# Performance work log

Measured on AMD Instinct MI355X. Metric: run time of the kernel, lower is better.

Reference implementation:

```python
import jax, jax.numpy as jnp
import numpy as np

B, S, E, H = 2, 2048, 1024, 8
DH = E // H          # v head dim = 128
F = DH // 2          # q/k sub-head dim = 64


def setup_inputs() -> dict:
    key = jax.random.key(0)
    ks = jax.random.split(key, 7)
    sc = E ** -0.5
    return {
        "x": jax.random.normal(ks[0], (B, S, E), dtype=jnp.float32),
        "Wq": jax.random.normal(ks[1], (E, E), dtype=jnp.float32) * sc,
        "Wk": jax.random.normal(ks[2], (E, E), dtype=jnp.float32) * sc,
        "Wv": jax.random.normal(ks[3], (E, E), dtype=jnp.float32) * sc,
        "norm_w": jnp.ones((H, DH), dtype=jnp.float32),
        "Wo": jax.random.normal(ks[4], (E, E), dtype=jnp.float32) * sc,
        "bo": jnp.zeros((E,), dtype=jnp.float32),
        "diff_weight": jnp.float32(0.2),
    }


def reference(x, Wq, Wk, Wv, norm_w, Wo, bo, diff_weight):
    b, s, e = x.shape
    # projections (Linear with weight [out,in] -> x @ W.T)
    qs = (x @ Wq.T).reshape(b, s, H, 2, F)
    ks_ = (x @ Wk.T).reshape(b, s, H, 2, F)
    vs = (x @ Wv.T).reshape(b, s, H, DH)
    scale = F ** -0.5
    # two attention branches: [2, b, h, q, k]
    scores = jnp.einsum('bqhif,bkhif->ibhqk', qs, ks_) * scale
    atts = jax.nn.softmax(scores, axis=-1)
    att = atts[0] - diff_weight * atts[1]          # [b,h,q,k]
    o = jnp.einsum('bhqk,bkhe->bqhe', att, vs)     # [b,q,h,dh]
    # RMSNorm over the joint (heads, head_dim) dims, as in nn.RMSNorm([H, DH])
    eps = jnp.finfo(o.dtype).eps
    rms = jax.lax.rsqrt(jnp.mean(o * o, axis=(-2, -1), keepdims=True) + eps)
    normed = (o * rms * norm_w).reshape(b, s, e)
    return (normed @ Wo.T + bo) * (1.0 - diff_weight)
```

## Files before the change

### kernel.cpp

```cpp
#include <hip/hip_runtime.h>
#include <hip/hip_bf16.h>
#include <math.h>


#define SDIM 2048
#define EDIM 1024
#define HDIM 8
#define DHDIM 128

typedef unsigned short u16;
typedef __attribute__((ext_vector_type(8))) short bf16x8;
typedef __attribute__((ext_vector_type(4))) short bf16x4;
typedef __attribute__((ext_vector_type(4))) u16 u16x4;
typedef __attribute__((ext_vector_type(8))) u16 u16x8;
typedef __attribute__((ext_vector_type(4))) float f32x4;

__device__ __forceinline__ u16 bf16rne(float f) {
    unsigned int u = __float_as_uint(f);
    u += 0x7fff + ((u >> 16) & 1);
    return (u16)(u >> 16);
}

__device__ __forceinline__ void gload16(void* lds, const void* g) {
    __builtin_amdgcn_global_load_lds(
        (const __attribute__((address_space(1))) unsigned int*)g,
        (__attribute__((address_space(3))) unsigned int*)lds, 16, 0, 0);
}

constexpr int GM = 4096, GN = 1024, GK = 1024;

__global__ __launch_bounds__(256) void cast_bf16(
    const float* __restrict__ x,  const float* __restrict__ wq,
    const float* __restrict__ wk, const float* __restrict__ wv,
    const float* __restrict__ wo,
    u16* __restrict__ xb,  u16* __restrict__ wqb, u16* __restrict__ wkb,
    u16* __restrict__ wvb, u16* __restrict__ wob)
{
    int bid = blockIdx.x;
    const float* src; u16* dst; int lb;
    if (bid < 2048)      { src = x;  dst = xb;  lb = bid; }
    else if (bid < 2560) { src = wq; dst = wqb; lb = bid - 2048; }
    else if (bid < 3072) { src = wk; dst = wkb; lb = bid - 2560; }
    else if (bid < 3584) { src = wv; dst = wvb; lb = bid - 3072; }
    else                 { src = wo; dst = wob; lb = bid - 3584; }
    size_t i = ((size_t)lb * 256 + threadIdx.x) * 8;
    float4 a = *(const float4*)&src[i];
    float4 b = *(const float4*)&src[i + 4];
    u16x8 o;
    o[0] = bf16rne(a.x); o[1] = bf16rne(a.y); o[2] = bf16rne(a.z); o[3] = bf16rne(a.w);
    o[4] = bf16rne(b.x); o[5] = bf16rne(b.y); o[6] = bf16rne(b.z); o[7] = bf16rne(b.w);
    *(u16x8*)&dst[i] = o;
}

struct GemmCore {
    f32x4 acc[4][4];
    int m0, n0, wm, wn, ln, quad;
};

__device__ __forceinline__ void gemm_swz(GemmCore& g) {
    const int bid = blockIdx.y * gridDim.x + blockIdx.x;
    const int cpx = (gridDim.x * gridDim.y) >> 3;
    const int swz = (bid & 7) * cpx + (bid >> 3);
    g.m0 = (swz / gridDim.x) * 128;
    g.n0 = (swz % gridDim.x) * 128;
}

#define QBUF 4096

__device__ __forceinline__ void gemm_core32(
    GemmCore& g, const u16* __restrict__ A, const u16* __restrict__ W,
    u16* AsBase, u16* BsBase)
{
    const int tid = threadIdx.x;
    const int lane = tid & 63;
    const int wv = tid >> 6;
    g.ln = lane & 15; g.quad = lane >> 4;
    g.wm = (wv >> 1) * 64; g.wn = (wv & 1) * 64;
    gemm_swz(g);

#pragma unroll
    for (int i = 0; i < 4; ++i)
#pragma unroll
        for (int j = 0; j < 4; ++j)
            g.acc[i][j] = (f32x4){0.f, 0.f, 0.f, 0.f};

    const int s0 = tid, s1 = tid + 256;
    const int ar0 = s0 >> 2, ac0 = (((s0 & 3) ^ ((ar0 >> 1) & 3)) * 8);
    const int ar1 = s1 >> 2, ac1 = (((s1 & 3) ^ ((ar1 >> 1) & 3)) * 8);
    const u16* pa0 = A + (size_t)(g.m0 + ar0) * GK + ac0;
    const u16* pa1 = A + (size_t)(g.m0 + ar1) * GK + ac1;
    const u16* pb0 = W + (size_t)(g.n0 + ar0) * GK + ac0;
    const u16* pb1 = W + (size_t)(g.n0 + ar1) * GK + ac1;
    u16* la0 = AsBase + s0 * 8; u16* la1 = AsBase + s1 * 8;
    u16* lb0 = BsBase + s0 * 8; u16* lb1 = BsBase + s1 * 8;

    const int roff = ((g.quad ^ ((g.ln >> 1) & 3)) * 8);

    gload16(la0, pa0); gload16(la1, pa1);
    gload16(lb0, pb0); gload16(lb1, pb1);

    for (int k0 = 0; k0 < GK; k0 += 32) {
        const int cur = (k0 >> 5) & 1;
        __syncthreads();

        if (k0 + 32 < GK) {
            const int nb = (cur ^ 1) * QBUF;
            gload16(la0 + nb, pa0 + k0 + 32); gload16(la1 + nb, pa1 + k0 + 32);
            gload16(lb0 + nb, pb0 + k0 + 32); gload16(lb1 + nb, pb1 + k0 + 32);
        }

        const u16* Ac = AsBase + cur * QBUF;
        const u16* Bc = BsBase + cur * QBUF;

        bf16x8 af[4], bfr[4];
#pragma unroll
        for (int t = 0; t < 4; ++t) {
            af[t]  = *(const bf16x8*)&Ac[(g.wm + t * 16 + g.ln) * 32 + roff];
            bfr[t] = *(const bf16x8*)&Bc[(g.wn + t * 16 + g.ln) * 32 + roff];
        }
#pragma unroll
        for (int i = 0; i < 4; ++i)
#pragma unroll
            for (int j = 0; j < 4; ++j)
                g.acc[i][j] = __builtin_amdgcn_mfma_f32_16x16x32_bf16(
                    af[i], bfr[j], g.acc[i][j], 0, 0, 0);
    }
}

#define GBUF 8192

__device__ __forceinline__ void gemm_core64(
    GemmCore& g, const u16* __restrict__ A, const u16* __restrict__ W,
    u16* AsBase, u16* BsBase)
{
    const int tid = threadIdx.x;
    const int lane = tid & 63;
    const int wv = tid >> 6;
    g.ln = lane & 15; g.quad = lane >> 4;
    g.wm = (wv >> 1) * 64; g.wn = (wv & 1) * 64;
    gemm_swz(g);

#pragma unroll
    for (int i = 0; i < 4; ++i)
#pragma unroll
        for (int j = 0; j < 4; ++j)
            g.acc[i][j] = (f32x4){0.f, 0.f, 0.f, 0.f};

    const int s0 = tid, s1 = tid + 256, s2 = tid + 512, s3 = tid + 768;
    const int ar0 = s0 >> 3, ac0 = ((s0 & 7) ^ (ar0 & 7)) * 8;
    const int ar1 = s1 >> 3, ac1 = ((s1 & 7) ^ (ar1 & 7)) * 8;
    const int ar2 = s2 >> 3, ac2 = ((s2 & 7) ^ (ar2 & 7)) * 8;
    const int ar3 = s3 >> 3, ac3 = ((s3 & 7) ^ (ar3 & 7)) * 8;
    const u16* pa0 = A + (size_t)(g.m0 + ar0) * GK + ac0;
    const u16* pa1 = A + (size_t)(g.m0 + ar1) * GK + ac1;
    const u16* pa2 = A + (size_t)(g.m0 + ar2) * GK + ac2;
    const u16* pa3 = A + (size_t)(g.m0 + ar3) * GK + ac3;
    const u16* pb0 = W + (size_t)(g.n0 + ar0) * GK + ac0;
    const u16* pb1 = W + (size_t)(g.n0 + ar1) * GK + ac1;
    const u16* pb2 = W + (size_t)(g.n0 + ar2) * GK + ac2;
    const u16* pb3 = W + (size_t)(g.n0 + ar3) * GK + ac3;
    u16* la0 = AsBase + s0 * 8; u16* la1 = AsBase + s1 * 8;
    u16* la2 = AsBase + s2 * 8; u16* la3 = AsBase + s3 * 8;
    u16* lb0 = BsBase + s0 * 8; u16* lb1 = BsBase + s1 * 8;
    u16* lb2 = BsBase + s2 * 8; u16* lb3 = BsBase + s3 * 8;

    gload16(la0, pa0); gload16(la1, pa1);
    gload16(la2, pa2); gload16(la3, pa3);
    gload16(lb0, pb0); gload16(lb1, pb1);
    gload16(lb2, pb2); gload16(lb3, pb3);

    for (int k0 = 0; k0 < GK; k0 += 64) {
        const int cur = (k0 >> 6) & 1;
        __syncthreads();

        if (k0 + 64 < GK) {
            const int nb = (cur ^ 1) * GBUF;
            gload16(la0 + nb, pa0 + k0 + 64); gload16(la1 + nb, pa1 + k0 + 64);
            gload16(la2 + nb, pa2 + k0 + 64); gload16(la3 + nb, pa3 + k0 + 64);
            gload16(lb0 + nb, pb0 + k0 + 64); gload16(lb1 + nb, pb1 + k0 + 64);
            gload16(lb2 + nb, pb2 + k0 + 64); gload16(lb3 + nb, pb3 + k0 + 64);
        }

        const u16* Ac = AsBase + cur * GBUF;
        const u16* Bc = BsBase + cur * GBUF;

        bf16x8 af[4][2], bfr[4][2];
#pragma unroll
        for (int t = 0; t < 4; ++t) {
#pragma unroll
            for (int kk = 0; kk < 2; ++kk) {
                const int ra = g.wm + t * 16 + g.ln;
                const int rb = g.wn + t * 16 + g.ln;
                af[t][kk]  = *(const bf16x8*)&Ac[ra * 64 + (((kk * 4 + g.quad) ^ (ra & 7)) * 8)];
                bfr[t][kk] = *(const bf16x8*)&Bc[rb * 64 + (((kk * 4 + g.quad) ^ (rb & 7)) * 8)];
            }
        }
#pragma unroll
        for (int i = 0; i < 4; ++i)
#pragma unroll
            for (int j = 0; j < 4; ++j)
#pragma unroll
                for (int kk = 0; kk < 2; ++kk)
                    g.acc[i][j] = __builtin_amdgcn_mfma_f32_16x16x32_bf16(
                        af[i][kk], bfr[j][kk], g.acc[i][j], 0, 0, 0);
    }
}

#define TSTR 136

__global__ __launch_bounds__(256) void gemm_qkv(
    const u16* __restrict__ A,
    const u16* __restrict__ W0, const u16* __restrict__ W1, const u16* __restrict__ W2,
    u16* __restrict__ Qb, u16* __restrict__ Kb, u16* __restrict__ Vtb)
{
    __shared__ u16 Sh[17408];
    const int z = blockIdx.z;
    const u16* W = (z == 0) ? W0 : ((z == 1) ? W1 : W2);
    GemmCore g;
    gemm_core32(g, A, W, Sh, Sh + 2 * QBUF);

    if (z < 2) {
        const float scl = (z == 0) ? 0.125f * 1.44269504f : 1.0f;
        u16* C = (z == 0) ? Qb : Kb;
#pragma unroll
        for (int i = 0; i < 4; ++i) {
            int rb = g.m0 + g.wm + i * 16 + g.quad * 4;
#pragma unroll
            for (int r = 0; r < 4; ++r) {
                u16* crow = C + (size_t)(rb + r) * GN + g.n0 + g.wn + g.ln;
#pragma unroll
                for (int j = 0; j < 4; ++j)
                    crow[j * 16] = bf16rne(g.acc[i][j][r] * scl);
            }
        }
    } else {
        __syncthreads();
        u16* Ts = Sh;
#pragma unroll
        for (int i = 0; i < 4; ++i)
#pragma unroll
            for (int j = 0; j < 4; ++j) {
                const int nl = g.wn + j * 16 + g.ln;
                const int ml = g.wm + i * 16 + g.quad * 4;
                u16x4 pk;
#pragma unroll
                for (int r = 0; r < 4; ++r) pk[r] = bf16rne(g.acc[i][j][r]);
                *(u16x4*)&Ts[nl * TSTR + ml] = pk;
            }
        __syncthreads();

        const int tid = threadIdx.x;
        const int c = tid & 15;
        const int bb = g.m0 >> 11;
        const int sb0 = g.m0 & 2047;
        const int hh = g.n0 >> 7;
#pragma unroll
        for (int s = 0; s < 8; ++s) {
            const int rown = (tid >> 4) + s * 16;
            u16x8 v = *(const u16x8*)&Ts[rown * TSTR + c * 8];
            u16* vrow = Vtb + (((size_t)bb * 8 + hh) * DHDIM + rown) * SDIM + sb0;
            *(u16x8*)&vrow[c * 8] = v;
        }
    }
}

__global__ __launch_bounds__(256) void gemm_out(
    const u16* __restrict__ A, const u16* __restrict__ W,
    float* __restrict__ C, const float* __restrict__ bias,
    const float* __restrict__ dwp)
{
    __shared__ u16 Sh[4 * GBUF];
    GemmCore g;
    gemm_core64(g, A, W, Sh, Sh + 2 * GBUF);

    const float scale = 1.0f - dwp[0];
    float bv[4];
#pragma unroll
    for (int j = 0; j < 4; ++j) bv[j] = bias[g.n0 + g.wn + j * 16 + g.ln];
#pragma unroll
    for (int i = 0; i < 4; ++i) {
        int rb = g.m0 + g.wm + i * 16 + g.quad * 4;
#pragma unroll
        for (int r = 0; r < 4; ++r) {
            float* crow = C + (size_t)(rb + r) * GN + g.n0 + g.wn + g.ln;
#pragma unroll
            for (int j = 0; j < 4; ++j)
                crow[j * 16] = (g.acc[i][j][r] + bv[j]) * scale;
        }
    }
}

#define KBUF 4096
#define VBUF 8192

__global__ __launch_bounds__(256, 2) void attn_mfma(
    const u16* __restrict__ Qb, const u16* __restrict__ Kb,
    const u16* __restrict__ Vtb,
    float* __restrict__ Oacc, float* __restrict__ Lacc)
{
    __shared__ u16 Ks[2 * KBUF];
    __shared__ u16 Vs[2 * VBUF];

    const int tid = threadIdx.x;
    const int wv   = tid >> 6;
    const int lane = tid & 63;
    const int ln = lane & 15, quad = lane >> 4;
    const int lx = ln & 7;
    const int vkey = (ln >> 1) & 3;
    const int bh = blockIdx.y, b = bh >> 3, h = bh & 7;
    const int q0 = blockIdx.x * 128 + wv * 32;
    const int BR = blockIdx.z;

    const size_t qoff = (size_t)b * SDIM * EDIM + h * DHDIM + BR * 64;
    bf16x8 aq[2][2];
#pragma unroll
    for (int qt = 0; qt < 2; ++qt) {
        const u16* qp = Qb + qoff + (size_t)(q0 + qt * 16 + ln) * EDIM + quad * 8;
        aq[qt][0] = *(const bf16x8*)(qp);
        aq[qt][1] = *(const bf16x8*)(qp + 32);
    }

    const int s0 = tid, s1 = tid + 256;
    const int kr0 = s0 >> 3, kc0 = ((s0 & 7) ^ (kr0 & 7)) * 8;
    const int kr1 = s1 >> 3, kc1 = ((s1 & 7) ^ (kr1 & 7)) * 8;
    const u16* kg0 = Kb + (size_t)(b * SDIM + kr0) * EDIM + h * DHDIM + BR * 64 + kc0;
    const u16* kg1 = Kb + (size_t)(b * SDIM + kr1) * EDIM + h * DHDIM + BR * 64 + kc1;
    const int vr0 = s0 >> 2, vc0 = ((s0 & 3) ^ ((vr0 >> 1) & 3)) * 8;
    const int vr1 = s1 >> 2, vc1 = ((s1 & 3) ^ ((vr1 >> 1) & 3)) * 8;
    const u16* vg0 = Vtb + ((size_t)bh * DHDIM + vr0) * SDIM + vc0;
    const u16* vg1 = Vtb + ((size_t)bh * DHDIM + vr1) * SDIM + vc1;
    u16* ksd0 = Ks + s0 * 8; u16* ksd1 = Ks + s1 * 8;
    u16* vsd0 = Vs + s0 * 8; u16* vsd1 = Vs + s1 * 8;

    gload16(ksd0, kg0); gload16(ksd1, kg1);
    gload16(vsd0, vg0); gload16(vsd1, vg1);
    gload16(vsd0 + 4096, vg0 + 32); gload16(vsd1 + 4096, vg1 + 32);
    kg0 += 64 * EDIM; kg1 += 64 * EDIM; vg0 += 64; vg1 += 64;

    f32x4 acc[2][8];
#pragma unroll
    for (int qt = 0; qt < 2; ++qt)
#pragma unroll
        for (int d = 0; d < 8; ++d)
            acc[qt][d] = (f32x4){0.f, 0.f, 0.f, 0.f};
    float lsum[2] = {0.f, 0.f};
    const f32x4 z4 = (f32x4){0.f, 0.f, 0.f, 0.f};

    for (int it = 0; it < 32; ++it) {
        const int cur = it & 1;
        __syncthreads();

        if (it < 31) {
            const int kb = (cur ^ 1) * KBUF, vb2 = (cur ^ 1) * VBUF;
            gload16(ksd0 + kb, kg0); gload16(ksd1 + kb, kg1);
            gload16(vsd0 + vb2, vg0); gload16(vsd1 + vb2, vg1);
            gload16(vsd0 + vb2 + 4096, vg0 + 32); gload16(vsd1 + vb2 + 4096, vg1 + 32);
            kg0 += 64 * EDIM; kg1 += 64 * EDIM; vg0 += 64; vg1 += 64;
        }

        const u16* Kc = Ks + cur * KBUF;
        const u16* Vc = Vs + cur * VBUF;

        bf16x8 kf[4][2];
#pragma unroll
        for (int t2 = 0; t2 < 4; ++t2) {
            const int rb = (t2 * 16 + ln) * 64;
            kf[t2][0] = *(const bf16x8*)&Kc[rb + ((quad ^ lx) * 8)];
            kf[t2][1] = *(const bf16x8*)&Kc[rb + (((4 + quad) ^ lx) * 8)];
        }

        f32x4 st[2][4];
#pragma unroll
        for (int t2 = 0; t2 < 4; ++t2)
#pragma unroll
            for (int qt = 0; qt < 2; ++qt) {
                f32x4 s = __builtin_amdgcn_mfma_f32_16x16x32_bf16(kf[t2][0], aq[qt][0], z4, 0, 0, 0);
                st[qt][t2] = __builtin_amdgcn_mfma_f32_16x16x32_bf16(kf[t2][1], aq[qt][1], s, 0, 0, 0);
            }

        bf16x8 vf[8][2];
#pragma unroll
        for (int dt = 0; dt < 8; ++dt) {
            const int vb = (dt * 16 + ln) * 32;
#pragma unroll
            for (int ks = 0; ks < 2; ++ks) {
                const u16* Vk = Vc + ks * 4096;
                bf16x4 vlo = *(const bf16x4*)&Vk[vb + ((((quad >> 1) + 0) ^ vkey) * 8 + (quad & 1) * 4)];
                bf16x4 vhi = *(const bf16x4*)&Vk[vb + ((((quad >> 1) + 2) ^ vkey) * 8 + (quad & 1) * 4)];
                vf[dt][ks] = __builtin_shufflevector(vlo, vhi, 0, 1, 2, 3, 4, 5, 6, 7);
            }
        }

        union { unsigned int u[4]; bf16x8 v; } ap[2][2];
#pragma unroll
        for (int qt = 0; qt < 2; ++qt)
#pragma unroll
            for (int ks = 0; ks < 2; ++ks) {
                float e0 = exp2f(st[qt][2 * ks][0]), e1 = exp2f(st[qt][2 * ks][1]);
                float e2 = exp2f(st[qt][2 * ks][2]), e3 = exp2f(st[qt][2 * ks][3]);
                float f0 = exp2f(st[qt][2 * ks + 1][0]), f1 = exp2f(st[qt][2 * ks + 1][1]);
                float f2 = exp2f(st[qt][2 * ks + 1][2]), f3 = exp2f(st[qt][2 * ks + 1][3]);
                lsum[qt] += (e0 + e1) + (e2 + e3) + (f0 + f1) + (f2 + f3);
                ap[qt][ks].u[0] = __builtin_amdgcn_perm(__float_as_uint(e1), __float_as_uint(e0), 0x07060302u);
                ap[qt][ks].u[1] = __builtin_amdgcn_perm(__float_as_uint(e3), __float_as_uint(e2), 0x07060302u);
                ap[qt][ks].u[2] = __builtin_amdgcn_perm(__float_as_uint(f1), __float_as_uint(f0), 0x07060302u);
                ap[qt][ks].u[3] = __builtin_amdgcn_perm(__float_as_uint(f3), __float_as_uint(f2), 0x07060302u);
            }

#pragma unroll
        for (int dt = 0; dt < 8; ++dt)
#pragma unroll
            for (int ks = 0; ks < 2; ++ks)
#pragma unroll
                for (int qt = 0; qt < 2; ++qt)
                    acc[qt][dt] = __builtin_amdgcn_mfma_f32_16x16x32_bf16(ap[qt][ks].v, vf[dt][ks], acc[qt][dt], 0, 0, 0);
    }

#pragma unroll
    for (int qt = 0; qt < 2; ++qt) {
#pragma unroll
        for (int r = 0; r < 4; ++r) {
            size_t row = (size_t)(b * SDIM + q0 + qt * 16 + quad * 4 + r);
            float* o = Oacc + ((row * 8 + h) * 2 + BR) * 128 + ln;
#pragma unroll
            for (int dt = 0; dt < 8; ++dt)
                o[dt * 16] = acc[qt][dt][r];
        }
    }
#pragma unroll
    for (int qt = 0; qt < 2; ++qt) {
        float l = lsum[qt];
        l += __shfl_xor(l, 16, 64); l += __shfl_xor(l, 32, 64);
        if (quad == 0)
            Lacc[(size_t)((b * 8 + h) * 2 + BR) * SDIM + q0 + qt * 16 + ln] = l;
    }
}

__global__ __launch_bounds__(256) void rms_combine(
    const float* __restrict__ Oacc, const float* __restrict__ Lacc,
    const float* __restrict__ nw, u16* __restrict__ Nb,
    const float* __restrict__ dwp)
{
    const int row = blockIdx.x;
    const int tid = threadIdx.x;
    const int h = tid >> 5, dh0 = (tid & 31) * 4;
    const int b = row >> 11, q = row & 2047;

    size_t ob = ((size_t)row * 8 + h) * 2 * 128;
    f32x4 a0 = *(const f32x4*)&Oacc[ob + dh0];
    f32x4 a1 = *(const f32x4*)&Oacc[ob + 128 + dh0];
    float l0 = Lacc[(size_t)((b * 8 + h) * 2 + 0) * SDIM + q];
    float l1 = Lacc[(size_t)((b * 8 + h) * 2 + 1) * SDIM + q];
    const float dw = dwp[0];
    float inv0 = 1.0f / l0;
    float inv1 = dw / l1;
    float o[4];
#pragma unroll
    for (int k = 0; k < 4; ++k) o[k] = a0[k] * inv0 - a1[k] * inv1;

    float ss = o[0] * o[0] + o[1] * o[1] + o[2] * o[2] + o[3] * o[3];
    ss += __shfl_xor(ss, 1,  64);
    ss += __shfl_xor(ss, 2,  64);
    ss += __shfl_xor(ss, 4,  64);
    ss += __shfl_xor(ss, 8,  64);
    ss += __shfl_xor(ss, 16, 64);
    ss += __shfl_xor(ss, 32, 64);
    __shared__ float red[4];
    if ((tid & 63) == 0) red[tid >> 6] = ss;
    __syncthreads();
    float tot = red[0] + red[1] + red[2] + red[3];
    float rms = rsqrtf(tot * (1.0f / 1024.0f) + 1.1920929e-07f);

    float4 w = *(const float4*)&nw[tid * 4];
    u16x4 pk;
    pk[0] = bf16rne(o[0] * rms * w.x);
    pk[1] = bf16rne(o[1] * rms * w.y);
    pk[2] = bf16rne(o[2] * rms * w.z);
    pk[3] = bf16rne(o[3] * rms * w.w);
    *(u16x4*)&Nb[(size_t)row * EDIM + tid * 4] = pk;
}

extern "C" void kernel_launch(void* const* d_in, const int* in_sizes, int n_in,
                              void* d_out, int out_size, void* d_ws, size_t ws_size,
                              hipStream_t stream)
{
    const float* x   = (const float*)d_in[0];
    const float* Wq  = (const float*)d_in[1];
    const float* Wk  = (const float*)d_in[2];
    const float* Wv  = (const float*)d_in[3];
    const float* nw  = (const float*)d_in[4];
    const float* Wo  = (const float*)d_in[5];
    const float* bo  = (const float*)d_in[6];
    const float* dwp = (const float*)d_in[7];
    float* out = (float*)d_out;

    float* Oacc = (float*)d_ws;
    u16*  xb   = (u16*)d_ws;
    u16*  wob  = (u16*)((char*)d_ws + 33554432);
    u16*  wqb  = wob + 1048576;
    u16*  wkb  = wqb + 1048576;
    u16*  wvb  = wkb + 1048576;
    float* Lacc = (float*)wqb;
    u16*  Qb   = wvb + 1048576;
    u16*  Kb   = Qb + 4194304;
    u16*  Vtb  = Kb + 4194304;
    u16*  Nb   = Qb;

    cast_bf16<<<4096, 256, 0, stream>>>(x, Wq, Wk, Wv, Wo,
                                        xb, wqb, wkb, wvb, wob);
    gemm_qkv<<<dim3(GN / 128, GM / 128, 3), 256, 0, stream>>>(
        xb, wqb, wkb, wvb, Qb, Kb, Vtb);
    attn_mfma<<<dim3(SDIM / 128, 2 * HDIM, 2), 256, 0, stream>>>(
        Qb, Kb, Vtb, Oacc, Lacc);
    rms_combine<<<4096, 256, 0, stream>>>(Oacc, Lacc, nw, Nb, dwp);
    gemm_out<<<dim3(GN / 128, GM / 128, 1), 256, 0, stream>>>(
        Nb, wob, out, bo, dwp);
}
```

Before: 212.9 us.

## Fuse fp32-to-bf16 cast of x into QKV GEMM A-tile loading

Drops the separate bf16 cast of the activation x. The QKV GEMM now reads fp32 x directly through registers, converts it, and stores bf16 into LDS with software prefetch across the MFMA loop. This removes one pass of writing and re-reading x as bf16. In exchange, each of the 3 z-slices and every N-tile re-reads fp32 x at twice the bytes, and the A loads lose the async global-to-LDS path.

```diff
diff --git a/kernel.cpp b/kernel.cpp
--- a/kernel.cpp
+++ b/kernel.cpp
@@ -27,29 +27,31 @@
         (__attribute__((address_space(3))) unsigned int*)lds, 16, 0, 0);
 }
 
+__device__ __forceinline__ u16x8 cvt8(float4 a, float4 b) {
+    u16x8 o;
+    o[0] = bf16rne(a.x); o[1] = bf16rne(a.y); o[2] = bf16rne(a.z); o[3] = bf16rne(a.w);
+    o[4] = bf16rne(b.x); o[5] = bf16rne(b.y); o[6] = bf16rne(b.z); o[7] = bf16rne(b.w);
+    return o;
+}
+
 constexpr int GM = 4096, GN = 1024, GK = 1024;
 
 __global__ __launch_bounds__(256) void cast_bf16(
-    const float* __restrict__ x,  const float* __restrict__ wq,
-    const float* __restrict__ wk, const float* __restrict__ wv,
-    const float* __restrict__ wo,
-    u16* __restrict__ xb,  u16* __restrict__ wqb, u16* __restrict__ wkb,
+    const float* __restrict__ wq, const float* __restrict__ wk,
+    const float* __restrict__ wv, const float* __restrict__ wo,
+    u16* __restrict__ wqb, u16* __restrict__ wkb,
     u16* __restrict__ wvb, u16* __restrict__ wob)
 {
     int bid = blockIdx.x;
     const float* src; u16* dst; int lb;
-    if (bid < 2048)      { src = x;  dst = xb;  lb = bid; }
-    else if (bid < 2560) { src = wq; dst = wqb; lb = bid - 2048; }
-    else if (bid < 3072) { src = wk; dst = wkb; lb = bid - 2560; }
-    else if (bid < 3584) { src = wv; dst = wvb; lb = bid - 3072; }
-    else                 { src = wo; dst = wob; lb = bid - 3584; }
+    if (bid < 512)       { src = wq; dst = wqb; lb = bid; }
+    else if (bid < 1024) { src = wk; dst = wkb; lb = bid - 512; }
+    else if (bid < 1536) { src = wv; dst = wvb; lb = bid - 1024; }
+    else                 { src = wo; dst = wob; lb = bid - 1536; }
     size_t i = ((size_t)lb * 256 + threadIdx.x) * 8;
     float4 a = *(const float4*)&src[i];
     float4 b = *(const float4*)&src[i + 4];
-    u16x8 o;
-    o[0] = bf16rne(a.x); o[1] = bf16rne(a.y); o[2] = bf16rne(a.z); o[3] = bf16rne(a.w);
-    o[4] = bf16rne(b.x); o[5] = bf16rne(b.y); o[6] = bf16rne(b.z); o[7] = bf16rne(b.w);
-    *(u16x8*)&dst[i] = o;
+    *(u16x8*)&dst[i] = cvt8(a, b);
 }
 
 struct GemmCore {
@@ -67,8 +69,8 @@
 
 #define QBUF 4096
 
-__device__ __forceinline__ void gemm_core32(
-    GemmCore& g, const u16* __restrict__ A, const u16* __restrict__ W,
+__device__ __forceinline__ void gemm_core32f(
+    GemmCore& g, const float* __restrict__ X, const u16* __restrict__ W,
     u16* AsBase, u16* BsBase)
 {
     const int tid = threadIdx.x;
@@ -87,8 +89,8 @@
     const int s0 = tid, s1 = tid + 256;
     const int ar0 = s0 >> 2, ac0 = (((s0 & 3) ^ ((ar0 >> 1) & 3)) * 8);
     const int ar1 = s1 >> 2, ac1 = (((s1 & 3) ^ ((ar1 >> 1) & 3)) * 8);
-    const u16* pa0 = A + (size_t)(g.m0 + ar0) * GK + ac0;
-    const u16* pa1 = A + (size_t)(g.m0 + ar1) * GK + ac1;
+    const float* xa0 = X + (size_t)(g.m0 + ar0) * GK + ac0;
+    const float* xa1 = X + (size_t)(g.m0 + ar1) * GK + ac1;
     const u16* pb0 = W + (size_t)(g.n0 + ar0) * GK + ac0;
     const u16* pb1 = W + (size_t)(g.n0 + ar1) * GK + ac1;
     u16* la0 = AsBase + s0 * 8; u16* la1 = AsBase + s1 * 8;
@@ -96,16 +98,28 @@
 
     const int roff = ((g.quad ^ ((g.ln >> 1) & 3)) * 8);
 
-    gload16(la0, pa0); gload16(la1, pa1);
+    {
+        float4 a0 = *(const float4*)(xa0);
+        float4 a1 = *(const float4*)(xa0 + 4);
+        float4 b0 = *(const float4*)(xa1);
+        float4 b1 = *(const float4*)(xa1 + 4);
+        *(u16x8*)la0 = cvt8(a0, a1);
+        *(u16x8*)la1 = cvt8(b0, b1);
+    }
     gload16(lb0, pb0); gload16(lb1, pb1);
 
     for (int k0 = 0; k0 < GK; k0 += 32) {
         const int cur = (k0 >> 5) & 1;
         __syncthreads();
 
-        if (k0 + 32 < GK) {
+        const bool pf = (k0 + 32 < GK);
+        float4 na0, na1, nb0l, nb1l;
+        if (pf) {
+            na0  = *(const float4*)(xa0 + k0 + 32);
+            na1  = *(const float4*)(xa0 + k0 + 36);
+            nb0l = *(const float4*)(xa1 + k0 + 32);
+            nb1l = *(const float4*)(xa1 + k0 + 36);
             const int nb = (cur ^ 1) * QBUF;
-            gload16(la0 + nb, pa0 + k0 + 32); gload16(la1 + nb, pa1 + k0 + 32);
             gload16(lb0 + nb, pb0 + k0 + 32); gload16(lb1 + nb, pb1 + k0 + 32);
         }
 
@@ -124,6 +138,12 @@
             for (int j = 0; j < 4; ++j)
                 g.acc[i][j] = __builtin_amdgcn_mfma_f32_16x16x32_bf16(
                     af[i], bfr[j], g.acc[i][j], 0, 0, 0);
+
+        if (pf) {
+            const int nb = (cur ^ 1) * QBUF;
+            *(u16x8*)(la0 + nb) = cvt8(na0, na1);
+            *(u16x8*)(la1 + nb) = cvt8(nb0l, nb1l);
+        }
     }
 }
 
@@ -209,7 +229,7 @@
 #define TSTR 136
 
 __global__ __launch_bounds__(256) void gemm_qkv(
-    const u16* __restrict__ A,
+    const float* __restrict__ X,
     const u16* __restrict__ W0, const u16* __restrict__ W1, const u16* __restrict__ W2,
     u16* __restrict__ Qb, u16* __restrict__ Kb, u16* __restrict__ Vtb)
 {
@@ -217,7 +237,7 @@
     const int z = blockIdx.z;
     const u16* W = (z == 0) ? W0 : ((z == 1) ? W1 : W2);
     GemmCore g;
-    gemm_core32(g, A, W, Sh, Sh + 2 * QBUF);
+    gemm_core32f(g, X, W, Sh, Sh + 2 * QBUF);
 
     if (z < 2) {
         const float scl = (z == 0) ? 0.125f * 1.44269504f : 1.0f;
@@ -495,7 +515,6 @@
     float* out = (float*)d_out;
 
     float* Oacc = (float*)d_ws;
-    u16*  xb   = (u16*)d_ws;
     u16*  wob  = (u16*)((char*)d_ws + 33554432);
     u16*  wqb  = wob + 1048576;
     u16*  wkb  = wqb + 1048576;
@@ -506,10 +525,10 @@
     u16*  Vtb  = Kb + 4194304;
     u16*  Nb   = Qb;
 
-    cast_bf16<<<4096, 256, 0, stream>>>(x, Wq, Wk, Wv, Wo,
-                                        xb, wqb, wkb, wvb, wob);
+    cast_bf16<<<2048, 256, 0, stream>>>(Wq, Wk, Wv, Wo,
+                                        wqb, wkb, wvb, wob);
     gemm_qkv<<<dim3(GN / 128, GM / 128, 3), 256, 0, stream>>>(
-        xb, wqb, wkb, wvb, Qb, Kb, Vtb);
+        x, wqb, wkb, wvb, Qb, Kb, Vtb);
     attn_mfma<<<dim3(SDIM / 128, 2 * HDIM, 2), 256, 0, stream>>>(
         Qb, Kb, Vtb, Oacc, Lacc);
     rms_combine<<<4096, 256, 0, stream>>>(Oacc, Lacc, nw, Nb, dwp);
```

New measurement: 236.0 us. +10.8%, slower.
